# Kernel tuning notes

Hardware: AMD Instinct MI355X
Metric: run time of the kernel (lower is better)

Reference implementation:

```python
import jax, jax.numpy as jnp
import numpy as np

TEMPERATURE = 0.07
MSE_WEIGHT = 0.5
SUPCON_WEIGHT = 1.0
EPS = 1e-12  # F.normalize default eps

P_POS = 4000
P_NEG = 4000
NVOX = 32768
FEAT = 128


def setup_inputs() -> dict:
    key = jax.random.key(0)
    k1, k2, k3, k4, k5 = jax.random.split(key, 5)
    Zs = jax.random.normal(k1, (1, FEAT, NVOX), dtype=jnp.float32)
    pos_idx = jax.random.randint(k2, (P_POS,), 0, NVOX, dtype=jnp.int32)
    neg_idx = jax.random.randint(k3, (P_NEG,), 0, NVOX, dtype=jnp.int32)
    feature_diff = jax.random.normal(k4, (1, FEAT, 32, 32, 32), dtype=jnp.float32)
    input_diff = jax.random.normal(k5, (1, FEAT, 32, 32, 32), dtype=jnp.float32)
    return {"Zs": Zs, "pos_idx": pos_idx, "neg_idx": neg_idx,
            "feature_diff": feature_diff, "input_diff": input_diff}


def _l2_normalize_rows(x):
    # F.normalize(x, dim=1): x / max(||x||_2, eps)
    n = jnp.sqrt(jnp.sum(x * x, axis=1, keepdims=True))
    return x / jnp.maximum(n, EPS)


def _supcon_loss(Zs, pos_idx, neg_idx):
    feats = Zs[0].T                                   # [Nvox, F]
    pixels = jnp.concatenate([feats[pos_idx], feats[neg_idx]], axis=0)  # [N, F]
    n = pixels.shape[0]
    labels = jnp.concatenate([jnp.ones((P_POS,), jnp.int32),
                              jnp.zeros((P_NEG,), jnp.int32)])
    pixels = _l2_normalize_rows(pixels)
    dot = jnp.matmul(pixels, pixels.T) / TEMPERATURE  # [N, N]
    dot = _l2_normalize_rows(dot)                     # row-normalize the NxN matrix
    expm = jnp.exp(dot)
    class_mask = (labels[:, None] == labels[None, :]) & ~jnp.eye(n, dtype=bool)
    pos_term = expm * class_mask
    pos_term = jnp.where(pos_term == 0, 1.0, pos_term)
    denom = jnp.sum(expm * ~class_mask, axis=1) - jnp.diagonal(expm)  # [N]
    full_term = jnp.log(pos_term) - jnp.log(denom)[None, :]
    return -(1.0 / n) * jnp.sum(full_term)


def reference(Zs, pos_idx, neg_idx, feature_diff, input_diff):
    supcon = _supcon_loss(Zs, pos_idx, neg_idx)
    mse = jnp.mean((feature_diff - input_diff) ** 2)
    return SUPCON_WEIGHT * supcon + MSE_WEIGHT * mse
```

## Files before the change

kernel.cpp:

```cpp
#include <hip/hip_runtime.h>
#include <hip/hip_bf16.h>
#include <math.h>

typedef unsigned short u16;
typedef float  f32x4  __attribute__((ext_vector_type(4)));
typedef __bf16 bf16x8 __attribute__((ext_vector_type(8)));

#define NPOS   4000
#define LDP    136
#define TILE_CH 2176
#define MSE_N  4194304
#define GATHER_B 256
#define MSE_B    512
#define TLD    132

__device__ __forceinline__ void load_lds16(const void* g, void* l) {
  __builtin_amdgcn_global_load_lds(
      (const __attribute__((address_space(1))) unsigned int*)g,
      (__attribute__((address_space(3))) unsigned int*)l, 16, 0, 0);
}

__device__ __forceinline__ float bf2f(u16 h) {
  unsigned u = ((unsigned)h) << 16;
  return __builtin_bit_cast(float, u);
}

struct Args {
  const float* Zs; const int* pos; const int* neg;
  const float4* fd; const float4* idf;
  u16* Pc; u16* Prow; float* Gpart; float* Spart; u16* Gb; float* S;
  float* qpos; float* qneg; float* sdpos; float* sdneg;
  float* msepart; float* out;
};

__global__ __launch_bounds__(256) void prep_k(Args a) {
  __shared__ __align__(16) float tile[128 * TLD];
  __shared__ int mlist[1024];
  __shared__ int mcnt;
  int blk = blockIdx.x, tid = threadIdx.x;
  int wave = tid >> 6, lane = tid & 63;
  if (blk < GATHER_B) {
    int v0 = blk << 7;
    if (tid == 0) mcnt = 0;
    __syncthreads();
    {
      int rq = tid >> 5;
      int c4 = (tid & 31) << 2;
      #pragma unroll
      for (int p = 0; p < 16; ++p) {
        int f = p * 8 + rq;
        float4 v = *(const float4*)(a.Zs + ((size_t)f << 15) + v0 + c4);
        *(float4*)&tile[f * TLD + c4] = v;
      }
    }
    for (int k = 0; k < 4000; k += 256) {
      int i = k + tid;
      if (i < 4000) {
        unsigned dp = (unsigned)(a.pos[i] - v0);
        if (dp < 128u) { int m = atomicAdd(&mcnt, 1); mlist[m] = (i << 7) | dp; }
        unsigned dn = (unsigned)(a.neg[i] - v0);
        if (dn < 128u) { int m = atomicAdd(&mcnt, 1); mlist[m] = ((4096 + i) << 7) | dn; }
      }
    }
    __syncthreads();
    int nm = mcnt;
    for (int m = wave; m < nm; m += 4) {
      int e = mlist[m];
      int col = e >> 7, lv = e & 127;
      float x0 = tile[lane * TLD + lv];
      float x1 = tile[(lane + 64) * TLD + lv];
      float s = x0 * x0 + x1 * x1;
      #pragma unroll
      for (int o = 1; o < 64; o <<= 1) s += __shfl_xor(s, o, 64);
      float inv = 1.0f / fmaxf(sqrtf(s), 1e-12f);
      __hip_bfloat16 h0 = __float2bfloat16(x0 * inv);
      __hip_bfloat16 h1 = __float2bfloat16(x1 * inv);
      u16 b0 = *(u16*)&h0, b1 = *(u16*)&h1;
      a.Prow[(size_t)col * LDP + lane]      = b0;
      a.Prow[(size_t)col * LDP + lane + 64] = b1;
      size_t cbase = (size_t)(col >> 7) * (128 * LDP) + (col & 127);
      a.Pc[cbase + (size_t)lane * LDP]        = b0;
      a.Pc[cbase + (size_t)(lane + 64) * LDP] = b1;
    }
  } else if (blk < GATHER_B + MSE_B) {
    int b = blk - GATHER_B;
    float ms = 0.f;
    for (int idx = b * 256 + tid; idx < MSE_N / 4; idx += MSE_B * 256) {
      float4 u = a.fd[idx], w = a.idf[idx];
      float dx = u.x - w.x, dy = u.y - w.y, dz = u.z - w.z, dv = u.w - w.w;
      ms += dx * dx + dy * dy + dz * dz + dv * dv;
    }
    #pragma unroll
    for (int o = 1; o < 64; o <<= 1) ms += __shfl_xor(ms, o, 64);
    __shared__ float red[4];
    if (lane == 0) red[wave] = ms;
    __syncthreads();
    if (tid == 0) a.msepart[b] = red[0] + red[1] + red[2] + red[3];
  } else {
    int ch = (blk == GATHER_B + MSE_B) ? 31 : 63;
    for (int e = tid; e < 128 * 96; e += 256) {
      int f = e / 96, c = 32 + e % 96;
      a.Pc[(size_t)ch * (128 * LDP) + (size_t)f * LDP + c] = 0;
    }
  }
}

__global__ __launch_bounds__(256) void syrk_k(Args a) {
  __shared__ __align__(16) u16 T0[128 * LDP];
  int blk = blockIdx.x, tid = threadIdx.x;
  int wave = tid >> 6, lane = tid & 63;
  int wm = (wave >> 1) << 6, wn = (wave & 1) << 6;
  int r = lane & 15, q = lane >> 4;
  f32x4 acc[4][4];
  #pragma unroll
  for (int x = 0; x < 4; ++x)
    #pragma unroll
    for (int y = 0; y < 4; ++y) {
      acc[x][y][0] = 0.f; acc[x][y][1] = 0.f; acc[x][y][2] = 0.f; acc[x][y][3] = 0.f;
    }
  const u16* g = a.Pc + (size_t)blk * (128 * LDP);
  #pragma unroll
  for (int k = 0; k < 9; ++k) {
    int cc = k * 256 + tid;
    if (cc < TILE_CH) load_lds16(g + cc * 8, &T0[cc * 8]);
  }
  __syncthreads();
  #pragma unroll
  for (int kk = 0; kk < 4; ++kk) {
    int k0 = kk * 32 + q * 8;
    bf16x8 af[4], bfr[4];
    #pragma unroll
    for (int t = 0; t < 4; ++t) {
      af[t]  = *(const bf16x8*)&T0[(wm + t * 16 + r) * LDP + k0];
      bfr[t] = *(const bf16x8*)&T0[(wn + t * 16 + r) * LDP + k0];
    }
    #pragma unroll
    for (int mt = 0; mt < 4; ++mt)
      #pragma unroll
      for (int nt = 0; nt < 4; ++nt)
        acc[mt][nt] = __builtin_amdgcn_mfma_f32_16x16x32_bf16(
            af[mt], bfr[nt], acc[mt][nt], 0, 0, 0);
  }
  {
    int sf = tid >> 1, sh = tid & 1;
    float ssum = 0.f;
    const u16* base = &T0[sf * LDP + sh * 64];
    #pragma unroll
    for (int vb = 0; vb < 8; ++vb) {
      bf16x8 v = *(const bf16x8*)&base[vb * 8];
      #pragma unroll
      for (int j = 0; j < 8; ++j) ssum += (float)v[j];
    }
    ssum += __shfl_xor(ssum, 1, 64);
    if (sh == 0) a.Spart[blk * 128 + sf] = ssum;
  }
  float* Gp = a.Gpart + (size_t)blk * 16384;
  #pragma unroll
  for (int mt = 0; mt < 4; ++mt)
    #pragma unroll
    for (int nt = 0; nt < 4; ++nt)
      #pragma unroll
      for (int reg = 0; reg < 4; ++reg) {
        int ar = wm + mt * 16 + q * 4 + reg;
        int bc = wn + nt * 16 + r;
        Gp[ar * 128 + bc] = acc[mt][nt][reg];
      }
}

__global__ __launch_bounds__(256) void reduce_k(Args a) {
  int blk = blockIdx.x, tid = threadIdx.x;
  if (blk < 64) {
    int set = blk >> 5, f0 = (blk & 31) * 4;
    #pragma unroll
    for (int j = 0; j < 2; ++j) {
      int o = j * 256 + tid;
      int row = f0 + (o >> 7), col = o & 127;
      const float* src = a.Gpart + (size_t)set * 32 * 16384 + row * 128 + col;
      float s = 0.f;
      #pragma unroll
      for (int ch = 0; ch < 32; ++ch) s += src[(size_t)ch * 16384];
      __hip_bfloat16 h = __float2bfloat16(s);
      a.Gb[(size_t)set * (128 * LDP) + row * LDP + col] = *(u16*)&h;
    }
  } else {
    int set = tid >> 7, f = tid & 127;
    const float* sp = a.Spart + (size_t)set * 32 * 128 + f;
    float s = 0.f;
    #pragma unroll
    for (int ch = 0; ch < 32; ++ch) s += sp[ch * 128];
    a.S[tid] = s;
  }
}

__global__ __launch_bounds__(256) void quad_k(Args a) {
  __shared__ __align__(16) u16 T0[128 * LDP];
  __shared__ __align__(16) u16 T1[128 * LDP];
  __shared__ float Sl[256];
  __shared__ float qld[2][128];
  int cb = blockIdx.x & 63, set = blockIdx.x >> 6, tid = threadIdx.x;
  Sl[tid] = a.S[tid];
  const u16* gP = a.Prow + (size_t)cb * (128 * LDP);
  #pragma unroll
  for (int k = 0; k < 9; ++k) {
    int cc = k * 256 + tid;
    if (cc < TILE_CH) load_lds16(gP + cc * 8, &T1[cc * 8]);
  }
  const u16* gG = a.Gb + (size_t)set * (128 * LDP);
  #pragma unroll
  for (int k = 0; k < 9; ++k) {
    int cc = k * 256 + tid;
    if (cc < TILE_CH) load_lds16(gG + cc * 8, &T0[cc * 8]);
  }
  __syncthreads();
  int wave = tid >> 6, lane = tid & 63;
  int wm = (wave >> 1) << 6, wn = (wave & 1) << 6;
  int r = lane & 15, q = lane >> 4;
  f32x4 acc[4][4];
  #pragma unroll
  for (int x = 0; x < 4; ++x)
    #pragma unroll
    for (int y = 0; y < 4; ++y) {
      acc[x][y][0] = 0.f; acc[x][y][1] = 0.f; acc[x][y][2] = 0.f; acc[x][y][3] = 0.f;
    }
  #pragma unroll
  for (int kk = 0; kk < 4; ++kk) {
    int k0 = kk * 32 + q * 8;
    bf16x8 af[4], bfr[4];
    #pragma unroll
    for (int t = 0; t < 4; ++t) {
      af[t]  = *(const bf16x8*)&T0[(wm + t * 16 + r) * LDP + k0];
      bfr[t] = *(const bf16x8*)&T1[(wn + t * 16 + r) * LDP + k0];
    }
    #pragma unroll
    for (int mt = 0; mt < 4; ++mt)
      #pragma unroll
      for (int nt = 0; nt < 4; ++nt)
        acc[mt][nt] = __builtin_amdgcn_mfma_f32_16x16x32_bf16(
            af[mt], bfr[nt], acc[mt][nt], 0, 0, 0);
  }
  float qv[4] = {0.f, 0.f, 0.f, 0.f};
  #pragma unroll
  for (int nt = 0; nt < 4; ++nt) {
    int il = wn + nt * 16 + r;
    #pragma unroll
    for (int mt = 0; mt < 4; ++mt) {
      const u16* pp = &T1[il * LDP + wm + mt * 16 + q * 4];
      #pragma unroll
      for (int reg = 0; reg < 4; ++reg)
        qv[nt] += acc[mt][nt][reg] * bf2f(pp[reg]);
    }
  }
  #pragma unroll
  for (int nt = 0; nt < 4; ++nt) {
    qv[nt] += __shfl_xor(qv[nt], 16, 64);
    qv[nt] += __shfl_xor(qv[nt], 32, 64);
  }
  int half = wm >> 6;
  if (q == 0) {
    #pragma unroll
    for (int nt = 0; nt < 4; ++nt) qld[half][wn + nt * 16 + r] = qv[nt];
  }
  __syncthreads();
  float* qarr = set ? a.qneg : a.qpos;
  if (tid < 128) qarr[cb * 128 + tid] = qld[0][tid] + qld[1][tid];
  if (set == 0) {
    int which = tid >> 7, sl = tid & 127;
    const float* Sv = &Sl[which * 128];
    float d = 0.f;
    #pragma unroll
    for (int fb = 0; fb < 16; ++fb) {
      const u16* pv = &T1[sl * LDP + fb * 8];
      #pragma unroll
      for (int j = 0; j < 8; ++j) d += Sv[fb * 8 + j] * bf2f(pv[j]);
    }
    (which ? a.sdneg : a.sdpos)[cb * 128 + sl] = d;
  }
}

__global__ __launch_bounds__(256) void final_k(Args a) {
  int tid = threadIdx.x;
  int wave = tid >> 6, lane = tid & 63;
  float lg = 0.f, sm = 0.f;
  for (int col = tid; col < 8192; col += 256) {
    bool isp = col < NPOS;
    bool isn = (col >= 4096) && (col < 4096 + NPOS);
    if (isp || isn) {
      float qp = a.qpos[col], qn = a.qneg[col];
      float c = 1.0f / sqrtf(qp + qn);
      float qo  = isp ? qn : qp;
      float sdo = isp ? a.sdneg[col] : a.sdpos[col];
      float sds = isp ? a.sdpos[col] : a.sdneg[col];
      float denom = 4000.0f + c * sdo + 0.5f * c * c * qo;
      lg += logf(denom);
      sm += c * (sds - 1.0f);
    }
  }
  float ms = a.msepart[tid] + a.msepart[tid + 256];
  #pragma unroll
  for (int o = 1; o < 64; o <<= 1) {
    lg += __shfl_xor(lg, o, 64);
    sm += __shfl_xor(sm, o, 64);
    ms += __shfl_xor(ms, o, 64);
  }
  __shared__ float redf[12];
  if (lane == 0) { redf[wave] = lg; redf[4 + wave] = sm; redf[8 + wave] = ms; }
  __syncthreads();
  if (tid == 0) {
    float lgs = redf[0] + redf[1] + redf[2] + redf[3];
    float sms = redf[4] + redf[5] + redf[6] + redf[7];
    float mss = redf[8] + redf[9] + redf[10] + redf[11];
    a.out[0] = lgs - sms * (1.0f / 8000.0f) + 0.5f * (mss * (1.0f / (float)MSE_N));
  }
}

extern "C" void kernel_launch(void* const* d_in, const int* in_sizes, int n_in,
                              void* d_out, int out_size, void* d_ws, size_t ws_size,
                              hipStream_t stream) {
  char* ws = (char*)d_ws;
  Args args;
  args.Zs  = (const float*)d_in[0];
  args.pos = (const int*)d_in[1];
  args.neg = (const int*)d_in[2];
  args.fd  = (const float4*)d_in[3];
  args.idf = (const float4*)d_in[4];
  args.out = (float*)d_out;

  args.Pc      = (u16*)(ws + 0);
  args.Prow    = (u16*)(ws + 2228224);
  args.Gpart   = (float*)(ws + 4456448);
  args.Spart   = (float*)(ws + 8650752);
  args.Gb      = (u16*)(ws + 8683520);
  args.S       = (float*)(ws + 8753152);
  args.qpos    = (float*)(ws + 8754176);
  args.qneg    = (float*)(ws + 8786944);
  args.sdpos   = (float*)(ws + 8819712);
  args.sdneg   = (float*)(ws + 8852480);
  args.msepart = (float*)(ws + 8885248);

  prep_k<<<GATHER_B + MSE_B + 2, 256, 0, stream>>>(args);
  syrk_k<<<64, 256, 0, stream>>>(args);
  reduce_k<<<65, 256, 0, stream>>>(args);
  quad_k<<<128, 256, 0, stream>>>(args);
  final_k<<<1, 256, 0, stream>>>(args);
}
```

Measured before the change: 128.1 us.

## Move MSE reduction into syrk launch and fuse final reduction via last-block atomic

Moves the MSE partial-sum blocks out of the gather/prep kernel and into the syrk launch, so the memory-bound MSE stream runs alongside the matrix-multiply blocks. The MSE block count drops from 512 to 192. The separate single-block final kernel is removed. Its work now runs in the last quad_k block, found with a threadfence plus an atomic counter that prep_k resets. This saves one kernel launch and overlaps independent work, at the cost of atomic and fence overhead and fewer MSE blocks.

After: 139.7 us. 9.0% more time.

```diff
diff --git a/kernel.cpp b/kernel.cpp
--- a/kernel.cpp
+++ b/kernel.cpp
@@ -11,7 +11,7 @@
 #define TILE_CH 2176
 #define MSE_N  4194304
 #define GATHER_B 256
-#define MSE_B    512
+#define MSE_B    192
 #define TLD    132
 
 __device__ __forceinline__ void load_lds16(const void* g, void* l) {
@@ -30,7 +30,7 @@
   const float4* fd; const float4* idf;
   u16* Pc; u16* Prow; float* Gpart; float* Spart; u16* Gb; float* S;
   float* qpos; float* qneg; float* sdpos; float* sdneg;
-  float* msepart; float* out;
+  float* msepart; unsigned* qcnt; float* out;
 };
 
 __global__ __launch_bounds__(256) void prep_k(Args a) {
@@ -82,8 +82,22 @@
       a.Pc[cbase + (size_t)lane * LDP]        = b0;
       a.Pc[cbase + (size_t)(lane + 64) * LDP] = b1;
     }
-  } else if (blk < GATHER_B + MSE_B) {
-    int b = blk - GATHER_B;
+  } else {
+    int ch = (blk == GATHER_B) ? 31 : 63;
+    if (blk == GATHER_B && tid == 0) *a.qcnt = 0u;
+    for (int e = tid; e < 128 * 96; e += 256) {
+      int f = e / 96, c = 32 + e % 96;
+      a.Pc[(size_t)ch * (128 * LDP) + (size_t)f * LDP + c] = 0;
+    }
+  }
+}
+
+__global__ __launch_bounds__(256) void work_k(Args a) {
+  __shared__ __align__(16) u16 T0[128 * LDP];
+  int blk = blockIdx.x, tid = threadIdx.x;
+  int wave = tid >> 6, lane = tid & 63;
+  if (blk >= 64) {
+    int b = blk - 64;
     float ms = 0.f;
     for (int idx = b * 256 + tid; idx < MSE_N / 4; idx += MSE_B * 256) {
       float4 u = a.fd[idx], w = a.idf[idx];
@@ -96,19 +110,8 @@
     if (lane == 0) red[wave] = ms;
     __syncthreads();
     if (tid == 0) a.msepart[b] = red[0] + red[1] + red[2] + red[3];
-  } else {
-    int ch = (blk == GATHER_B + MSE_B) ? 31 : 63;
-    for (int e = tid; e < 128 * 96; e += 256) {
-      int f = e / 96, c = 32 + e % 96;
-      a.Pc[(size_t)ch * (128 * LDP) + (size_t)f * LDP + c] = 0;
-    }
-  }
-}
-
-__global__ __launch_bounds__(256) void syrk_k(Args a) {
-  __shared__ __align__(16) u16 T0[128 * LDP];
-  int blk = blockIdx.x, tid = threadIdx.x;
-  int wave = tid >> 6, lane = tid & 63;
+    return;
+  }
   int wm = (wave >> 1) << 6, wn = (wave & 1) << 6;
   int r = lane & 15, q = lane >> 4;
   f32x4 acc[4][4];
@@ -275,11 +278,14 @@
     }
     (which ? a.sdneg : a.sdpos)[cb * 128 + sl] = d;
   }
-}
-
-__global__ __launch_bounds__(256) void final_k(Args a) {
-  int tid = threadIdx.x;
-  int wave = tid >> 6, lane = tid & 63;
+  __threadfence();
+  __syncthreads();
+  __shared__ unsigned lastv;
+  if (tid == 0) lastv = atomicAdd(a.qcnt, 1u);
+  __syncthreads();
+  if (lastv != 127u) return;
+  __threadfence();
+  int wv = tid >> 6, lane2 = tid & 63;
   float lg = 0.f, sm = 0.f;
   for (int col = tid; col < 8192; col += 256) {
     bool isp = col < NPOS;
@@ -295,7 +301,7 @@
       sm += c * (sds - 1.0f);
     }
   }
-  float ms = a.msepart[tid] + a.msepart[tid + 256];
+  float ms = (tid < MSE_B) ? a.msepart[tid] : 0.f;
   #pragma unroll
   for (int o = 1; o < 64; o <<= 1) {
     lg += __shfl_xor(lg, o, 64);
@@ -303,7 +309,7 @@
     ms += __shfl_xor(ms, o, 64);
   }
   __shared__ float redf[12];
-  if (lane == 0) { redf[wave] = lg; redf[4 + wave] = sm; redf[8 + wave] = ms; }
+  if (lane2 == 0) { redf[wv] = lg; redf[4 + wv] = sm; redf[8 + wv] = ms; }
   __syncthreads();
   if (tid == 0) {
     float lgs = redf[0] + redf[1] + redf[2] + redf[3];
@@ -336,10 +342,10 @@
   args.sdpos   = (float*)(ws + 8819712);
   args.sdneg   = (float*)(ws + 8852480);
   args.msepart = (float*)(ws + 8885248);
-
-  prep_k<<<GATHER_B + MSE_B + 2, 256, 0, stream>>>(args);
-  syrk_k<<<64, 256, 0, stream>>>(args);
+  args.qcnt    = (unsigned*)(ws + 8886016);
+
+  prep_k<<<GATHER_B + 2, 256, 0, stream>>>(args);
+  work_k<<<64 + MSE_B, 256, 0, stream>>>(args);
   reduce_k<<<65, 256, 0, stream>>>(args);
   quad_k<<<128, 256, 0, stream>>>(args);
-  final_k<<<1, 256, 0, stream>>>(args);
-}
+}
```

## Fuse syrk, reduce, quad and final kernels into one persistent kernel with grid barriers

Applied to the files above, without the earlier changes.

Merges four launches into a single 128-block kernel. Software grid barriers built on atomic counters separate the partial Gram, reduction and quadratic-form phases, and a last-block-done counter runs the final reduction. The Prow tile is prefetched into LDS before the first barrier. This removes three kernel launch gaps, at the cost of spin-wait barriers that rely on all 128 blocks being co-resident.

Result: slower. 198.5 us (+55.0%).

```diff
diff --git a/kernel.cpp b/kernel.cpp
--- a/kernel.cpp
+++ b/kernel.cpp
@@ -30,8 +30,27 @@
   const float4* fd; const float4* idf;
   u16* Pc; u16* Prow; float* Gpart; float* Spart; u16* Gb; float* S;
   float* qpos; float* qneg; float* sdpos; float* sdneg;
-  float* msepart; float* out;
+  float* msepart; unsigned* qcnt; unsigned* bar; unsigned* gen; float* out;
 };
+
+__device__ __forceinline__ void gridbar(unsigned* bar, unsigned* gen, unsigned nb) {
+  __syncthreads();
+  __threadfence();
+  if (threadIdx.x == 0) {
+    unsigned g = __hip_atomic_load(gen, __ATOMIC_RELAXED, __HIP_MEMORY_SCOPE_AGENT);
+    unsigned prev = __hip_atomic_fetch_add(bar, 1u, __ATOMIC_ACQ_REL, __HIP_MEMORY_SCOPE_AGENT);
+    if (prev == nb - 1u) {
+      __hip_atomic_store(bar, 0u, __ATOMIC_RELAXED, __HIP_MEMORY_SCOPE_AGENT);
+      __hip_atomic_fetch_add(gen, 1u, __ATOMIC_RELEASE, __HIP_MEMORY_SCOPE_AGENT);
+    } else {
+      while (__hip_atomic_load(gen, __ATOMIC_ACQUIRE, __HIP_MEMORY_SCOPE_AGENT) == g) {
+        __builtin_amdgcn_s_sleep(2);
+      }
+    }
+  }
+  __syncthreads();
+  __threadfence();
+}
 
 __global__ __launch_bounds__(256) void prep_k(Args a) {
   __shared__ __align__(16) float tile[128 * TLD];
@@ -98,6 +117,9 @@
     if (tid == 0) a.msepart[b] = red[0] + red[1] + red[2] + red[3];
   } else {
     int ch = (blk == GATHER_B + MSE_B) ? 31 : 63;
+    if (blk == GATHER_B + MSE_B && tid == 0) {
+      *a.qcnt = 0u; *a.bar = 0u; *a.gen = 0u;
+    }
     for (int e = tid; e < 128 * 96; e += 256) {
       int f = e / 96, c = 32 + e % 96;
       a.Pc[(size_t)ch * (128 * LDP) + (size_t)f * LDP + c] = 0;
@@ -105,117 +127,117 @@
   }
 }
 
-__global__ __launch_bounds__(256) void syrk_k(Args a) {
-  __shared__ __align__(16) u16 T0[128 * LDP];
-  int blk = blockIdx.x, tid = threadIdx.x;
-  int wave = tid >> 6, lane = tid & 63;
-  int wm = (wave >> 1) << 6, wn = (wave & 1) << 6;
-  int r = lane & 15, q = lane >> 4;
-  f32x4 acc[4][4];
-  #pragma unroll
-  for (int x = 0; x < 4; ++x)
-    #pragma unroll
-    for (int y = 0; y < 4; ++y) {
-      acc[x][y][0] = 0.f; acc[x][y][1] = 0.f; acc[x][y][2] = 0.f; acc[x][y][3] = 0.f;
-    }
-  const u16* g = a.Pc + (size_t)blk * (128 * LDP);
-  #pragma unroll
-  for (int k = 0; k < 9; ++k) {
-    int cc = k * 256 + tid;
-    if (cc < TILE_CH) load_lds16(g + cc * 8, &T0[cc * 8]);
-  }
-  __syncthreads();
-  #pragma unroll
-  for (int kk = 0; kk < 4; ++kk) {
-    int k0 = kk * 32 + q * 8;
-    bf16x8 af[4], bfr[4];
-    #pragma unroll
-    for (int t = 0; t < 4; ++t) {
-      af[t]  = *(const bf16x8*)&T0[(wm + t * 16 + r) * LDP + k0];
-      bfr[t] = *(const bf16x8*)&T0[(wn + t * 16 + r) * LDP + k0];
-    }
-    #pragma unroll
-    for (int mt = 0; mt < 4; ++mt)
-      #pragma unroll
-      for (int nt = 0; nt < 4; ++nt)
-        acc[mt][nt] = __builtin_amdgcn_mfma_f32_16x16x32_bf16(
-            af[mt], bfr[nt], acc[mt][nt], 0, 0, 0);
-  }
-  {
-    int sf = tid >> 1, sh = tid & 1;
-    float ssum = 0.f;
-    const u16* base = &T0[sf * LDP + sh * 64];
-    #pragma unroll
-    for (int vb = 0; vb < 8; ++vb) {
-      bf16x8 v = *(const bf16x8*)&base[vb * 8];
-      #pragma unroll
-      for (int j = 0; j < 8; ++j) ssum += (float)v[j];
-    }
-    ssum += __shfl_xor(ssum, 1, 64);
-    if (sh == 0) a.Spart[blk * 128 + sf] = ssum;
-  }
-  float* Gp = a.Gpart + (size_t)blk * 16384;
-  #pragma unroll
-  for (int mt = 0; mt < 4; ++mt)
-    #pragma unroll
-    for (int nt = 0; nt < 4; ++nt)
-      #pragma unroll
-      for (int reg = 0; reg < 4; ++reg) {
-        int ar = wm + mt * 16 + q * 4 + reg;
-        int bc = wn + nt * 16 + r;
-        Gp[ar * 128 + bc] = acc[mt][nt][reg];
-      }
-}
-
-__global__ __launch_bounds__(256) void reduce_k(Args a) {
-  int blk = blockIdx.x, tid = threadIdx.x;
-  if (blk < 64) {
-    int set = blk >> 5, f0 = (blk & 31) * 4;
-    #pragma unroll
-    for (int j = 0; j < 2; ++j) {
-      int o = j * 256 + tid;
-      int row = f0 + (o >> 7), col = o & 127;
-      const float* src = a.Gpart + (size_t)set * 32 * 16384 + row * 128 + col;
-      float s = 0.f;
-      #pragma unroll
-      for (int ch = 0; ch < 32; ++ch) s += src[(size_t)ch * 16384];
-      __hip_bfloat16 h = __float2bfloat16(s);
-      a.Gb[(size_t)set * (128 * LDP) + row * LDP + col] = *(u16*)&h;
-    }
-  } else {
-    int set = tid >> 7, f = tid & 127;
-    const float* sp = a.Spart + (size_t)set * 32 * 128 + f;
-    float s = 0.f;
-    #pragma unroll
-    for (int ch = 0; ch < 32; ++ch) s += sp[ch * 128];
-    a.S[tid] = s;
-  }
-}
-
-__global__ __launch_bounds__(256) void quad_k(Args a) {
+__global__ __launch_bounds__(256) void mega_k(Args a) {
   __shared__ __align__(16) u16 T0[128 * LDP];
   __shared__ __align__(16) u16 T1[128 * LDP];
   __shared__ float Sl[256];
   __shared__ float qld[2][128];
-  int cb = blockIdx.x & 63, set = blockIdx.x >> 6, tid = threadIdx.x;
-  Sl[tid] = a.S[tid];
-  const u16* gP = a.Prow + (size_t)cb * (128 * LDP);
-  #pragma unroll
-  for (int k = 0; k < 9; ++k) {
-    int cc = k * 256 + tid;
-    if (cc < TILE_CH) load_lds16(gP + cc * 8, &T1[cc * 8]);
-  }
-  const u16* gG = a.Gb + (size_t)set * (128 * LDP);
-  #pragma unroll
-  for (int k = 0; k < 9; ++k) {
-    int cc = k * 256 + tid;
-    if (cc < TILE_CH) load_lds16(gG + cc * 8, &T0[cc * 8]);
-  }
-  __syncthreads();
+  int blk = blockIdx.x, tid = threadIdx.x;
   int wave = tid >> 6, lane = tid & 63;
+  int cb = blk & 63, set = blk >> 6;
   int wm = (wave >> 1) << 6, wn = (wave & 1) << 6;
   int r = lane & 15, q = lane >> 4;
+
+  {
+    const u16* gP = a.Prow + (size_t)cb * (128 * LDP);
+    #pragma unroll
+    for (int k = 0; k < 9; ++k) {
+      int cc = k * 256 + tid;
+      if (cc < TILE_CH) load_lds16(gP + cc * 8, &T1[cc * 8]);
+    }
+  }
+
   f32x4 acc[4][4];
+  if (blk < 64) {
+    #pragma unroll
+    for (int x = 0; x < 4; ++x)
+      #pragma unroll
+      for (int y = 0; y < 4; ++y) {
+        acc[x][y][0] = 0.f; acc[x][y][1] = 0.f; acc[x][y][2] = 0.f; acc[x][y][3] = 0.f;
+      }
+    const u16* g = a.Pc + (size_t)blk * (128 * LDP);
+    #pragma unroll
+    for (int k = 0; k < 9; ++k) {
+      int cc = k * 256 + tid;
+      if (cc < TILE_CH) load_lds16(g + cc * 8, &T0[cc * 8]);
+    }
+    __syncthreads();
+    #pragma unroll
+    for (int kk = 0; kk < 4; ++kk) {
+      int k0 = kk * 32 + q * 8;
+      bf16x8 af[4], bfr[4];
+      #pragma unroll
+      for (int t = 0; t < 4; ++t) {
+        af[t]  = *(const bf16x8*)&T0[(wm + t * 16 + r) * LDP + k0];
+        bfr[t] = *(const bf16x8*)&T0[(wn + t * 16 + r) * LDP + k0];
+      }
+      #pragma unroll
+      for (int mt = 0; mt < 4; ++mt)
+        #pragma unroll
+        for (int nt = 0; nt < 4; ++nt)
+          acc[mt][nt] = __builtin_amdgcn_mfma_f32_16x16x32_bf16(
+              af[mt], bfr[nt], acc[mt][nt], 0, 0, 0);
+    }
+    {
+      int sf = tid >> 1, sh = tid & 1;
+      float ssum = 0.f;
+      const u16* base = &T0[sf * LDP + sh * 64];
+      #pragma unroll
+      for (int vb = 0; vb < 8; ++vb) {
+        bf16x8 v = *(const bf16x8*)&base[vb * 8];
+        #pragma unroll
+        for (int j = 0; j < 8; ++j) ssum += (float)v[j];
+      }
+      ssum += __shfl_xor(ssum, 1, 64);
+      if (sh == 0) a.Spart[blk * 128 + sf] = ssum;
+    }
+    float* Gp = a.Gpart + (size_t)blk * 16384;
+    #pragma unroll
+    for (int mt = 0; mt < 4; ++mt)
+      #pragma unroll
+      for (int nt = 0; nt < 4; ++nt)
+        #pragma unroll
+        for (int reg = 0; reg < 4; ++reg) {
+          int ar = wm + mt * 16 + q * 4 + reg;
+          int bc = wn + nt * 16 + r;
+          Gp[ar * 128 + bc] = acc[mt][nt][reg];
+        }
+  }
+  gridbar(a.bar, a.gen, 128u);
+
+  if (blk < 64) {
+    int set_r = blk >> 5, f0 = (blk & 31) * 4;
+    #pragma unroll
+    for (int j = 0; j < 2; ++j) {
+      int o = j * 256 + tid;
+      int row = f0 + (o >> 7), col = o & 127;
+      const float* src = a.Gpart + (size_t)set_r * 32 * 16384 + row * 128 + col;
+      float s = 0.f;
+      #pragma unroll
+      for (int ch = 0; ch < 32; ++ch) s += src[(size_t)ch * 16384];
+      __hip_bfloat16 h = __float2bfloat16(s);
+      a.Gb[(size_t)set_r * (128 * LDP) + row * LDP + col] = *(u16*)&h;
+    }
+  } else if (blk == 64) {
+    int set_r = tid >> 7, f = tid & 127;
+    const float* sp = a.Spart + (size_t)set_r * 32 * 128 + f;
+    float s = 0.f;
+    #pragma unroll
+    for (int ch = 0; ch < 32; ++ch) s += sp[ch * 128];
+    a.S[tid] = s;
+  }
+  gridbar(a.bar, a.gen, 128u);
+
+  {
+    const u16* gG = a.Gb + (size_t)set * (128 * LDP);
+    #pragma unroll
+    for (int k = 0; k < 9; ++k) {
+      int cc = k * 256 + tid;
+      if (cc < TILE_CH) load_lds16(gG + cc * 8, &T0[cc * 8]);
+    }
+  }
+  Sl[tid] = a.S[tid];
+  __syncthreads();
   #pragma unroll
   for (int x = 0; x < 4; ++x)
     #pragma unroll
@@ -275,11 +297,15 @@
     }
     (which ? a.sdneg : a.sdpos)[cb * 128 + sl] = d;
   }
-}
-
-__global__ __launch_bounds__(256) void final_k(Args a) {
-  int tid = threadIdx.x;
-  int wave = tid >> 6, lane = tid & 63;
+
+  __threadfence();
+  __syncthreads();
+  __shared__ unsigned lastv;
+  if (tid == 0) lastv = atomicAdd(a.qcnt, 1u);
+  __syncthreads();
+  if (lastv != 127u) return;
+  __threadfence();
+  int wv = tid >> 6, lane2 = tid & 63;
   float lg = 0.f, sm = 0.f;
   for (int col = tid; col < 8192; col += 256) {
     bool isp = col < NPOS;
@@ -303,7 +329,7 @@
     ms += __shfl_xor(ms, o, 64);
   }
   __shared__ float redf[12];
-  if (lane == 0) { redf[wave] = lg; redf[4 + wave] = sm; redf[8 + wave] = ms; }
+  if (lane2 == 0) { redf[wv] = lg; redf[4 + wv] = sm; redf[8 + wv] = ms; }
   __syncthreads();
   if (tid == 0) {
     float lgs = redf[0] + redf[1] + redf[2] + redf[3];
@@ -336,10 +362,10 @@
   args.sdpos   = (float*)(ws + 8819712);
   args.sdneg   = (float*)(ws + 8852480);
   args.msepart = (float*)(ws + 8885248);
+  args.qcnt    = (unsigned*)(ws + 8887296);
+  args.bar     = (unsigned*)(ws + 8887300);
+  args.gen     = (unsigned*)(ws + 8887304);
 
   prep_k<<<GATHER_B + MSE_B + 2, 256, 0, stream>>>(args);
-  syrk_k<<<64, 256, 0, stream>>>(args);
-  reduce_k<<<65, 256, 0, stream>>>(args);
-  quad_k<<<128, 256, 0, stream>>>(args);
-  final_k<<<1, 256, 0, stream>>>(args);
-}
+  mega_k<<<128, 256, 0, stream>>>(args);
+}
```
